# Kernel tuning notes

Hardware: AMD Instinct MI355X
Metric: run time of the kernel (lower is better)

Reference implementation:

```python
import math
import jax, jax.numpy as jnp
import numpy as np


def _bilinear_maps_sample(kv_feats, shapes_wh, start_ids, locs, map_ids):
    """Bilinear sampling from concatenated multi-level 2D maps.

    kv_feats: [BH, S, C] flattened (row-major, per level) feature maps
    shapes_wh: [L, 2] int (W, H) per level
    start_ids: [L] int start offset of each level in S
    locs: [BH, M, 2] normalized (x, y) in [0, 1]
    map_ids: [BH, M] int level index per sample
    returns [BH, M, C]
    """
    wh = shapes_wh[map_ids]                      # [BH, M, 2]
    W = wh[..., 0]
    H = wh[..., 1]
    start = start_ids[map_ids]                   # [BH, M]
    Wf = W.astype(locs.dtype)
    Hf = H.astype(locs.dtype)
    x = locs[..., 0] * Wf - 0.5                  # align_corners=False convention
    y = locs[..., 1] * Hf - 0.5
    x0 = jnp.floor(x)
    y0 = jnp.floor(y)
    out = jnp.zeros(locs.shape[:-1] + (kv_feats.shape[-1],), kv_feats.dtype)
    for dx in (0, 1):
        for dy in (0, 1):
            xi = x0 + dx
            yi = y0 + dy
            w = (1.0 - jnp.abs(x - xi)) * (1.0 - jnp.abs(y - yi))
            valid = (xi >= 0) & (xi < Wf) & (yi >= 0) & (yi < Hf)
            xi_c = jnp.clip(xi, 0, Wf - 1).astype(jnp.int32)
            yi_c = jnp.clip(yi, 0, Hf - 1).astype(jnp.int32)
            idx = start + yi_c * W + xi_c        # [BH, M]
            f = jnp.take_along_axis(kv_feats, idx[..., None], axis=1)
            out = out + jnp.where(valid, w, 0.0)[..., None] * f
    return out


def setup_inputs() -> dict:
    key = jax.random.key(0)
    ks = jax.random.split(key, 10)
    B, N, L, Hh, P = 2, 2048, 5, 8, 4
    in_size, sample_size = 256, 256
    qk_size, value_size = 256, 256
    kv_size = qk_size + value_size

    shapes = np.array([[128, 128], [64, 64], [32, 32], [16, 16], [8, 8]], np.int32)  # (H, W)
    flat = (shapes[:, 0] * shapes[:, 1]).astype(np.int64)
    start = np.concatenate([[0], np.cumsum(flat)[:-1]]).astype(np.int32)
    S = int(flat.sum())  # 21824

    # sampling_offsets bias: canonical Deformable-DETR grid init
    thetas = np.arange(Hh, dtype=np.float32) * (2.0 * math.pi / Hh)
    grid = np.stack([np.cos(thetas), np.sin(thetas)], axis=1)
    grid = grid / np.abs(grid).max(axis=1, keepdims=True)
    grid = np.tile(grid.reshape(Hh, 1, 1, 2), (1, L, 1, 1))
    sizes = np.arange(1, P + 1, dtype=np.float32).reshape(1, 1, P, 1)
    b_off = (sizes * grid).reshape(-1)           # [H*L*P*2]

    def lin(k, out_d, in_d):
        return jax.random.normal(k, (out_d, in_d), jnp.float32) * (1.0 / math.sqrt(in_d))

    return {
        "in_feats": jax.random.normal(ks[0], (B, N, in_size), jnp.float32),
        "sample_priors": jax.random.uniform(ks[1], (B, N, L, 2), jnp.float32),
        "sample_feats": jax.random.normal(ks[2], (B, S, sample_size), jnp.float32),
        "sample_map_shapes": jnp.asarray(shapes),
        "sample_map_start_ids": jnp.asarray(start),
        "W_off": jax.random.normal(ks[3], (Hh * L * P * 2, in_size), jnp.float32) * 0.02,
        "b_off": jnp.asarray(b_off),
        "W_q": lin(ks[4], qk_size, in_size),
        "b_q": jnp.zeros((qk_size,), jnp.float32),
        "W_kv": lin(ks[5], kv_size, sample_size),
        "b_kv": jnp.zeros((kv_size,), jnp.float32),
        "point_encs": jax.random.normal(ks[6], (Hh, L * P, qk_size // Hh), jnp.float32) * 0.02,
        "W_out": lin(ks[7], in_size, value_size),
        "b_out": jnp.zeros((in_size,), jnp.float32),
    }


def reference(in_feats, sample_priors, sample_feats, sample_map_shapes,
              sample_map_start_ids, W_off, b_off, W_q, b_q, W_kv, b_kv,
              point_encs, W_out, b_out):
    B, N = in_feats.shape[:2]
    Hh, LP, dqk = point_encs.shape
    L = sample_map_shapes.shape[0]
    P = LP // L

    # sampling offsets + locations (priors last dim == 2 path)
    off = (in_feats @ W_off.T + b_off).reshape(B, N, Hh, L, P, 2)
    shapes_wh = sample_map_shapes[:, ::-1]                      # fliplr -> (W, H)
    norm = shapes_wh.astype(in_feats.dtype)[None, None, None, :, None, :]
    locs = sample_priors[:, :, None, :, None, :] + off / norm    # [B,N,H,L,P,2]

    q = (in_feats @ W_q.T + b_q).reshape(B, N, Hh, dqk)
    kv = sample_feats @ W_kv.T + b_kv                            # [B,S,kv_size]
    ck = kv.shape[-1] // Hh
    kv = kv.reshape(B, -1, Hh, ck).transpose(0, 2, 1, 3).reshape(B * Hh, -1, ck)

    locs = locs.transpose(0, 2, 1, 3, 4, 5).reshape(B * Hh, N * L * P, 2)
    map_ids = jnp.broadcast_to(jnp.arange(L, dtype=jnp.int32)[None, None, :, None],
                               (B * Hh, N, L, P)).reshape(B * Hh, -1)

    sampled = _bilinear_maps_sample(kv, shapes_wh, sample_map_start_ids, locs, map_ids)
    sampled = sampled.reshape(B, Hh, N, LP, ck).transpose(0, 2, 1, 3, 4)  # [B,N,H,LP,ck]

    keys = sampled[..., :dqk] + point_encs                       # [B,N,H,LP,dqk]
    vals = sampled[..., dqk:]                                    # [B,N,H,LP,cv]
    attn = jax.nn.softmax(
        jnp.einsum('bnhd,bnhpd->bnhp', q / math.sqrt(dqk), keys), axis=-1)
    weighted = jnp.einsum('bnhp,bnhpd->bnhd', attn, vals).reshape(B, N, -1)
    return weighted @ W_out.T + b_out
```

## Files before the change

kernel.cpp:

```cpp
#include <hip/hip_runtime.h>
#include <cstddef>

#define B_  2
#define N_  2048
#define L_  5
#define HH  8
#define P_  4
#define S_  21824
#define DQK 32

using bf16x8 = __attribute__((ext_vector_type(8))) short;
using f32x4  = __attribute__((ext_vector_type(4))) float;
using us8    = __attribute__((ext_vector_type(8))) unsigned short;
using h2     = __attribute__((ext_vector_type(2))) _Float16;

__device__ __forceinline__ unsigned short f2b(float f) {
  unsigned u = __builtin_bit_cast(unsigned, f);
  u += 0x7FFFu + ((u >> 16) & 1u);
  return (unsigned short)(u >> 16);
}
__device__ __forceinline__ float b2f(unsigned short h) {
  return __builtin_bit_cast(float, ((unsigned)h) << 16);
}
__device__ __forceinline__ unsigned cvtpk(float lo, float hi) {
  unsigned r;
  asm("v_cvt_pk_bf16_f32 %0, %1, %2" : "=v"(r) : "v"(lo), "v"(hi));
  return r;
}
__device__ __forceinline__ h2 pkrtz(float a, float b) {
  return __builtin_bit_cast(h2, __builtin_amdgcn_cvt_pkrtz(a, b));
}
__device__ __forceinline__ unsigned pkrtz_u(float a, float b) {
  return __builtin_bit_cast(unsigned, __builtin_amdgcn_cvt_pkrtz(a, b));
}
__device__ __forceinline__ h2 u2h(unsigned u) { return __builtin_bit_cast(h2, u); }

__device__ __forceinline__ void gld_lds16(const void* g, void* l) {
  __builtin_amdgcn_global_load_lds(
      (const __attribute__((address_space(1))) unsigned int*)g,
      (__attribute__((address_space(3))) unsigned int*)l, 16, 0, 0);
}

template <int CTRL>
__device__ __forceinline__ float dppadd(float v) {
  const int x = __builtin_bit_cast(int, v);
  return v + __builtin_bit_cast(float,
      __builtin_amdgcn_update_dpp(x, x, CTRL, 0xF, 0xF, false));
}

#define F0 131072
#define F1 147456
#define F2 155648
#define F3 163840
#define F4 176128
#define F5 188416

__device__ __forceinline__ void cvt8_plain(const float* s, unsigned short* d, int u) {
  const float4 a = ((const float4*)s)[2 * u];
  const float4 b = ((const float4*)s)[2 * u + 1];
  us8 o;
  o[0] = f2b(a.x); o[1] = f2b(a.y); o[2] = f2b(a.z); o[3] = f2b(a.w);
  o[4] = f2b(b.x); o[5] = f2b(b.y); o[6] = f2b(b.z); o[7] = f2b(b.w);
  ((us8*)d)[u] = o;
}
__device__ __forceinline__ unsigned short f2b_lo(float x) {
  return f2b(x - b2f(f2b(x)));
}
__device__ __forceinline__ void cvt8_lo(const float* s, unsigned short* d, int u) {
  const float4 a = ((const float4*)s)[2 * u];
  const float4 b = ((const float4*)s)[2 * u + 1];
  us8 o;
  o[0] = f2b_lo(a.x); o[1] = f2b_lo(a.y); o[2] = f2b_lo(a.z); o[3] = f2b_lo(a.w);
  o[4] = f2b_lo(b.x); o[5] = f2b_lo(b.y); o[6] = f2b_lo(b.z); o[7] = f2b_lo(b.w);
  ((us8*)d)[u] = o;
}
__device__ __forceinline__ void cvt8_both(const float* s, unsigned short* dh,
                                          unsigned short* dl, int u) {
  const float4 a = ((const float4*)s)[2 * u];
  const float4 b = ((const float4*)s)[2 * u + 1];
  us8 oh, ol;
  const float v[8] = {a.x, a.y, a.z, a.w, b.x, b.y, b.z, b.w};
#pragma unroll
  for (int k = 0; k < 8; ++k) {
    const unsigned short hh = f2b(v[k]);
    oh[k] = hh;
    ol[k] = f2b(v[k] - b2f(hh));
  }
  ((us8*)dh)[u] = oh;
  ((us8*)dl)[u] = ol;
}

__global__ __launch_bounds__(256) void cvt_all(
    const float* __restrict__ in_feats, const float* __restrict__ W_kv,
    const float* __restrict__ W_q, const float* __restrict__ W_out,
    const float* __restrict__ W_off,
    unsigned short* __restrict__ if_hi, unsigned short* __restrict__ if_lo,
    unsigned short* __restrict__ wkv_bf, unsigned short* __restrict__ wq_bf,
    unsigned short* __restrict__ wout_bf, unsigned short* __restrict__ woff_hi,
    unsigned short* __restrict__ woff_lo) {
  const int i = blockIdx.x * 256 + threadIdx.x;
  if      (i < F0) cvt8_both(in_feats, if_hi, if_lo, i);
  else if (i < F1) cvt8_plain(W_kv, wkv_bf, i - F0);
  else if (i < F2) cvt8_plain(W_q, wq_bf, i - F1);
  else if (i < F3) cvt8_plain(W_out, wout_bf, i - F2);
  else if (i < F4) {
    const int u = i - F3;
    if ((u >> 5) < 320) cvt8_plain(W_off, woff_hi, u);
    else ((us8*)woff_hi)[u] = (us8)0;
  } else {
    const int u = i - F4;
    if ((u >> 5) < 320) cvt8_lo(W_off, woff_lo, u);
    else ((us8*)woff_lo)[u] = (us8)0;
  }
}

__device__ __forceinline__ void mfma_compute(
    const unsigned short* As, const unsigned short* Bs,
    int wr, int wc, int fr, int fq, f32x4 (&acc)[4][4]) {
#pragma unroll
  for (int kk = 0; kk < 2; ++kk) {
    bf16x8 af[4], bfv[4];
#pragma unroll
    for (int i = 0; i < 4; ++i) {
      const int ar = wr * 64 + i * 16 + fr;
      const int cha = (kk * 4 + fq) ^ (ar & 7);
      af[i] = *(const bf16x8*)(As + ar * 64 + cha * 8);
      const int br = wc * 64 + i * 16 + fr;
      const int chb = (kk * 4 + fq) ^ (br & 7);
      bfv[i] = *(const bf16x8*)(Bs + br * 64 + chb * 8);
    }
#pragma unroll
    for (int i = 0; i < 4; ++i)
#pragma unroll
      for (int j = 0; j < 4; ++j)
        acc[i][j] = __builtin_amdgcn_mfma_f32_16x16x32_bf16(
            af[i], bfv[j], acc[i][j], 0, 0, 0);
  }
}

__device__ __forceinline__ void mfma_tile_bf16(
    const unsigned short* __restrict__ Ap, const unsigned short* __restrict__ Wp,
    unsigned short* As, unsigned short* Bs,
    int row0, int col0, int wv, int wr, int wc, int fr, int fq,
    int srow, int sch, f32x4 (&acc)[4][4]) {
  for (int k0 = 0; k0 < 256; k0 += 64) {
#pragma unroll
    for (int i = 0; i < 4; ++i) {
      const int r = i * 32 + srow;
      const int ca = sch ^ (r & 7);
      gld_lds16(Ap + (size_t)(row0 + r) * 256 + k0 + ca * 8,
                As + (size_t)(i * 32 + wv * 8) * 64);
      gld_lds16(Wp + (size_t)(col0 + r) * 256 + k0 + ca * 8,
                Bs + (size_t)(i * 32 + wv * 8) * 64);
    }
    __syncthreads();
    mfma_compute(As, Bs, wr, wc, fr, fq, acc);
    __syncthreads();
  }
}

__global__ __launch_bounds__(256) void ubergemm(
    const float* __restrict__ sfeats,
    const unsigned short* __restrict__ wkv_bf,
    const unsigned short* __restrict__ if_hi,
    const unsigned short* __restrict__ if_lo,
    const unsigned short* __restrict__ woff_hi,
    const unsigned short* __restrict__ woff_lo,
    const unsigned short* __restrict__ wq_bf,
    const float* __restrict__ b_kv, const float* __restrict__ b_off,
    const float* __restrict__ b_q,
    unsigned short* __restrict__ kvt, float* __restrict__ offb,
    float* __restrict__ qb) {
  __shared__ __align__(16) unsigned char ldsraw[49152];

  const int tid = threadIdx.x;
  const int lane = tid & 63;
  const int wv = tid >> 6;
  const int wr = wv >> 1, wc = wv & 1;
  const int fr = lane & 15, fq = lane >> 4;
  const int bx = blockIdx.x;

  f32x4 acc[4][4] = {};

  if (bx >= 160) {
    const int t = bx - 160;
    const int x = t & 7;
    const int idx = t >> 3;
    const int c = idx & 3;
    const int g = (idx >> 2) * 8 + x;
    if (g >= 341) return;
    const int row0 = g * 128;
    const int col0 = c * 128;

    float* Afb[2] = {(float*)ldsraw, (float*)(ldsraw + 16384)};
    unsigned short* Bb[2] = {(unsigned short*)(ldsraw + 32768),
                             (unsigned short*)(ldsraw + 40960)};

#define KV_STAGE(KK, BUF)                                                     \
    {                                                                         \
      _Pragma("unroll")                                                       \
      for (int ld = 0; ld < 4; ++ld) {             \
        const int ci = ld * 256 + tid;                                        \
        const int rw = ci >> 3, cc = ci & 7;                                  \
        const int ca = cc ^ (rw & 7);                                         \
        gld_lds16(sfeats + (size_t)(row0 + rw) * 256 + (KK) * 32 + ca * 4,    \
                  (char*)Afb[BUF] + (ld * 4096 + wv * 1024));                 \
      }                                                                       \
      _Pragma("unroll")                                                       \
      for (int ld = 0; ld < 2; ++ld) {              \
        const int ci = ld * 256 + tid;                                        \
        const int rw = ci >> 2, cc = ci & 3;                                  \
        const int ca = cc ^ ((rw >> 1) & 3);        \
        gld_lds16(wkv_bf + (size_t)(col0 + rw) * 256 + (KK) * 32 + ca * 8,    \
                  (char*)Bb[BUF] + (ld * 4096 + wv * 1024));                  \
      }                                                                       \
    }

    KV_STAGE(0, 0);
#pragma unroll
    for (int k = 0; k < 8; ++k) {
      if (k < 7) {
        KV_STAGE(k + 1, (k + 1) & 1);
        asm volatile("s_waitcnt vmcnt(6)" ::: "memory");
      } else {
        asm volatile("s_waitcnt vmcnt(0)" ::: "memory");
      }
      __builtin_amdgcn_s_barrier();
      __builtin_amdgcn_sched_barrier(0);
      const float* Ac = Afb[k & 1];
      const unsigned short* Bc = Bb[k & 1];
      bf16x8 af[4], bfv[4];
#pragma unroll
      for (int i = 0; i < 4; ++i) {
        const int ar = wr * 64 + i * 16 + fr;
        const int swz = ar & 7;
        const float4 a0 = *(const float4*)(Ac + ar * 32 + (((fq * 2) ^ swz) * 4));
        const float4 a1 = *(const float4*)(Ac + ar * 32 + (((fq * 2 + 1) ^ swz) * 4));
        uint4 u;
        u.x = cvtpk(a0.x, a0.y);
        u.y = cvtpk(a0.z, a0.w);
        u.z = cvtpk(a1.x, a1.y);
        u.w = cvtpk(a1.z, a1.w);
        af[i] = __builtin_bit_cast(bf16x8, u);
      }
#pragma unroll
      for (int j = 0; j < 4; ++j) {
        const int nr = wc * 64 + j * 16 + fr;
        bfv[j] = *(const bf16x8*)(Bc + (nr * 4 + (fq ^ ((nr >> 1) & 3))) * 8);
      }
      __builtin_amdgcn_s_setprio(1);
#pragma unroll
      for (int j = 0; j < 4; ++j)
#pragma unroll
        for (int i = 0; i < 4; ++i)
          acc[j][i] = __builtin_amdgcn_mfma_f32_16x16x32_bf16(
              bfv[j], af[i], acc[j][i], 0, 0, 0);
      __builtin_amdgcn_s_setprio(0);
      __builtin_amdgcn_s_barrier();
    }
#undef KV_STAGE

#pragma unroll
    for (int j = 0; j < 4; ++j) {
      const int c0 = col0 + wc * 64 + j * 16 + fq * 4;
      const float4 bb = *(const float4*)(b_kv + c0);
      const int h = c0 >> 6;
      const int cc = c0 & 63;
#pragma unroll
      for (int i = 0; i < 4; ++i) {
        const int sl = row0 + wr * 64 + i * 16 + fr;
        const int b = (sl >= S_) ? 1 : 0;
        const int s = sl - b * S_;
        unsigned* dst = (unsigned*)(kvt + ((size_t)(b * HH + h) * S_ + s) * 64 + cc);
        dst[0] = pkrtz_u(acc[j][i][0] + bb.x, acc[j][i][1] + bb.y);
        dst[1] = pkrtz_u(acc[j][i][2] + bb.z, acc[j][i][3] + bb.w);
      }
    }
    return;
  }

  unsigned short* As = (unsigned short*)ldsraw;
  unsigned short* Bs = (unsigned short*)(ldsraw + 16384);
  const int srow = tid >> 3;
  const int sch = tid & 7;
  int row0, col0, ldc, nbias;
  const float* bias;
  float* Cf;
  if (bx < 96) {
    col0 = (bx % 3) * 128; row0 = (bx / 3) * 128;
    bias = b_off; Cf = offb; ldc = 384; nbias = 320;
    mfma_tile_bf16(if_hi, woff_hi, As, Bs, row0, col0, wv, wr, wc, fr, fq, srow, sch, acc);
    mfma_tile_bf16(if_hi, woff_lo, As, Bs, row0, col0, wv, wr, wc, fr, fq, srow, sch, acc);
    mfma_tile_bf16(if_lo, woff_hi, As, Bs, row0, col0, wv, wr, wc, fr, fq, srow, sch, acc);
  } else {
    const int t = bx - 96;
    col0 = (t & 1) * 128; row0 = (t >> 1) * 128;
    bias = b_q; Cf = qb; ldc = 256; nbias = 256;
    mfma_tile_bf16(if_hi, wq_bf, As, Bs, row0, col0, wv, wr, wc, fr, fq, srow, sch, acc);
  }

#pragma unroll
  for (int j = 0; j < 4; ++j) {
    const int n = col0 + wc * 64 + j * 16 + fr;
    const float bv = (n < nbias) ? bias[n] : 0.f;
#pragma unroll
    for (int i = 0; i < 4; ++i) {
      const int mbase = row0 + wr * 64 + i * 16 + fq * 4;
#pragma unroll
      for (int r = 0; r < 4; ++r)
        Cf[(size_t)(mbase + r) * ldc + n] = acc[i][j][r] + bv;
    }
  }
}

__global__ __launch_bounds__(256) void gemm_out(
    const unsigned short* __restrict__ A, const unsigned short* __restrict__ Wt,
    const float* __restrict__ bias, float* __restrict__ C) {
  __shared__ __align__(16) unsigned short As[128 * 64];
  __shared__ __align__(16) unsigned short Bs[128 * 64];
  const int tid = threadIdx.x;
  const int lane = tid & 63;
  const int wv = tid >> 6;
  const int wr = wv >> 1, wc = wv & 1;
  const int fr = lane & 15, fq = lane >> 4;
  const int row0 = blockIdx.y * 128, col0 = blockIdx.x * 128;
  const int srow = tid >> 3, sch = tid & 7;
  f32x4 acc[4][4] = {};
  mfma_tile_bf16(A, Wt, As, Bs, row0, col0, wv, wr, wc, fr, fq, srow, sch, acc);
#pragma unroll
  for (int j = 0; j < 4; ++j) {
    const int n = col0 + wc * 64 + j * 16 + fr;
    const float bv = bias[n];
#pragma unroll
    for (int i = 0; i < 4; ++i) {
      const int mbase = row0 + wr * 64 + i * 16 + fq * 4;
#pragma unroll
      for (int r = 0; r < 4; ++r)
        C[(size_t)(mbase + r) * 256 + n] = acc[i][j][r] + bv;
    }
  }
}

__global__ __launch_bounds__(256) void sample_attn6(
    const unsigned short* __restrict__ kvt,
    const float* __restrict__ offb,
    const float* __restrict__ qb,
    const float* __restrict__ priors,
    const int* __restrict__ shapes,
    const int* __restrict__ starts,
    const float* __restrict__ pencs,
    unsigned short* __restrict__ wtd) {
  __shared__ __align__(16) int pbuf[4][20][8];
  const int wv = threadIdx.x >> 6;
  const int lane = threadIdx.x & 63;
  const int beta = blockIdx.x;
  const int sig = (beta & 7) * 2 + (beta >> 12);
  const int chunk = (beta >> 3) & 511;
  const int h = sig & 7;
  const int b = sig >> 3;
  const int bn = b * N_ + chunk * 4 + wv;
  const int j = lane & 31;
  const int half = lane >> 5;

  if (lane < 20) {
    const int pp = lane;
    const int l = pp >> 2;
    const float2 oxy = *(const float2*)(offb + (size_t)bn * 384 + h * 40 + pp * 2);
    const float2 pxy = *(const float2*)(priors + ((size_t)bn * 5 + l) * 2);
    const int Wd = shapes[l * 2 + 1];
    const int Hd = shapes[l * 2 + 0];
    const int st = starts[l];
    const float Wf = (float)Wd, Hf = (float)Hd;
    const float x = (pxy.x + oxy.x / Wf) * Wf - 0.5f;
    const float y = (pxy.y + oxy.y / Hf) * Hf - 0.5f;
    const float x0f = floorf(x), y0f = floorf(y);
    const float fx = x - x0f, fy = y - y0f;
    const int xi = (int)x0f, yi = (int)y0f;
    int a[4]; unsigned wpk[4];
#pragma unroll
    for (int dy = 0; dy < 2; ++dy)
#pragma unroll
      for (int dx = 0; dx < 2; ++dx) {
        const int xc = xi + dx, yc = yi + dy;
        const bool valid = (xc >= 0) & (xc < Wd) & (yc >= 0) & (yc < Hd);
        const float wt = (dx ? fx : 1.f - fx) * (dy ? fy : 1.f - fy);
        const float wm = valid ? wt : 0.f;
        const int xcc = min(max(xc, 0), Wd - 1);
        const int ycc = min(max(yc, 0), Hd - 1);
        a[dy * 2 + dx] = (st + ycc * Wd + xcc) * 32;
        wpk[dy * 2 + dx] = pkrtz_u(wm, wm);
      }
    *(int4*)&pbuf[wv][pp][0] = make_int4(a[0], a[1], a[2], a[3]);
    *(int4*)&pbuf[wv][pp][4] =
        make_int4((int)wpk[0], (int)wpk[1], (int)wpk[2], (int)wpk[3]);
  }

  const int jc = j & 15;
  float2 q2 = *(const float2*)(qb + (size_t)bn * 256 + h * DQK + 2 * jc);
  q2.x *= 0.17677669529663687f;
  q2.y *= 0.17677669529663687f;
  const h2 qpk = pkrtz(q2.x, q2.y);
  float qpe[10];
#pragma unroll
  for (int i = 0; i < 10; ++i) {
    const float2 pe = *(const float2*)(
        pencs + ((size_t)h * 20 + 2 * i + half) * DQK + 2 * jc);
    qpe[i] = q2.x * pe.x + q2.y * pe.y;
  }

  const unsigned* kvd = (const unsigned*)(kvt + (size_t)(b * HH + h) * (S_ * 64));

  uint4 wwp[5];
  unsigned g[5][4];
#pragma unroll
  for (int i = 0; i < 5; ++i) {
    const int4 aa = *(const int4*)&pbuf[wv][2 * i + half][0];
    wwp[i] = *(const uint4*)&pbuf[wv][2 * i + half][4];
    g[i][0] = kvd[(unsigned)aa.x + j];
    g[i][1] = kvd[(unsigned)aa.y + j];
    g[i][2] = kvd[(unsigned)aa.z + j];
    g[i][3] = kvd[(unsigned)aa.w + j];
  }

  h2 sam[10];
  float lg[10];
#pragma unroll
  for (int i = 0; i < 10; ++i) {
    const int s = i % 5;
    const uint4 wt = wwp[s];
    const unsigned g0 = g[s][0], g1 = g[s][1], g2 = g[s][2], g3 = g[s][3];
    if (i < 5) {
      const int4 aa = *(const int4*)&pbuf[wv][2 * (i + 5) + half][0];
      wwp[s] = *(const uint4*)&pbuf[wv][2 * (i + 5) + half][4];
      g[s][0] = kvd[(unsigned)aa.x + j];
      g[s][1] = kvd[(unsigned)aa.y + j];
      g[s][2] = kvd[(unsigned)aa.z + j];
      g[s][3] = kvd[(unsigned)aa.w + j];
    }
    h2 v = u2h(wt.x) * u2h(g0);
    v = u2h(wt.y) * u2h(g1) + v;
    v = u2h(wt.z) * u2h(g2) + v;
    v = u2h(wt.w) * u2h(g3) + v;
    sam[i] = v;
    float part = (j < 16) ? __builtin_amdgcn_fdot2(qpk, v, qpe[i], false) : 0.f;
    part = dppadd<0xB1>(part);
    part = dppadd<0x4E>(part);
    part = dppadd<0x124>(part);
    part = dppadd<0x128>(part);
    lg[i] = part + __shfl_xor(part, 16, 64);
  }

  float mx = lg[0];
#pragma unroll
  for (int i = 1; i < 10; ++i) mx = fmaxf(mx, lg[i]);
  mx = fmaxf(mx, __shfl_xor(mx, 32, 64));
  float se = 0.f;
#pragma unroll
  for (int i = 0; i < 10; ++i) {
    lg[i] = __expf(lg[i] - mx);
    se += lg[i];
  }
  se += __shfl_xor(se, 32, 64);
  const float inv = 1.f / se;

  float ax = 0.f, ay = 0.f;
#pragma unroll
  for (int i = 0; i < 10; ++i) {
    ax = fmaf(lg[i], (float)sam[i][0], ax);
    ay = fmaf(lg[i], (float)sam[i][1], ay);
  }
  ax += __shfl_xor(ax, 32, 64);
  ay += __shfl_xor(ay, 32, 64);

  if (half == 0 && j >= 16) {
    const unsigned u = (unsigned)f2b(ax * inv) | ((unsigned)f2b(ay * inv) << 16);
    ((unsigned*)wtd)[(size_t)bn * 128 + h * 16 + (j - 16)] = u;
  }
}

extern "C" void kernel_launch(void* const* d_in, const int* in_sizes, int n_in,
                              void* d_out, int out_size, void* d_ws, size_t ws_size,
                              hipStream_t stream) {
  const float* in_feats = (const float*)d_in[0];
  const float* priors   = (const float*)d_in[1];
  const float* sfeats   = (const float*)d_in[2];
  const int*   shapes   = (const int*)d_in[3];
  const int*   starts   = (const int*)d_in[4];
  const float* W_off    = (const float*)d_in[5];
  const float* b_off    = (const float*)d_in[6];
  const float* W_q      = (const float*)d_in[7];
  const float* b_q      = (const float*)d_in[8];
  const float* W_kv     = (const float*)d_in[9];
  const float* b_kv     = (const float*)d_in[10];
  const float* pencs    = (const float*)d_in[11];
  const float* W_out    = (const float*)d_in[12];
  const float* b_out    = (const float*)d_in[13];
  float* out = (float*)d_out;

  char* w = (char*)d_ws;
  unsigned short* kvt = (unsigned short*)w;
  w += (size_t)B_ * HH * S_ * 64 * 2;
  unsigned short* if_hi = (unsigned short*)w; w += (size_t)4096 * 256 * 2;
  unsigned short* if_lo = (unsigned short*)w; w += (size_t)4096 * 256 * 2;
  unsigned short* wkv_bf = (unsigned short*)w;  w += (size_t)512 * 256 * 2;
  unsigned short* wq_bf  = (unsigned short*)w;  w += (size_t)256 * 256 * 2;
  unsigned short* wout_bf = (unsigned short*)w; w += (size_t)256 * 256 * 2;
  unsigned short* woff_hi = (unsigned short*)w; w += (size_t)384 * 256 * 2;
  unsigned short* woff_lo = (unsigned short*)w; w += (size_t)384 * 256 * 2;
  float* offb = (float*)w;  w += (size_t)4096 * 384 * 4;
  float* qb   = (float*)w;  w += (size_t)4096 * 256 * 4;
  unsigned short* wtd_bf = (unsigned short*)w; w += (size_t)4096 * 256 * 2;

  cvt_all<<<F5 / 256, 256, 0, stream>>>(
      in_feats, W_kv, W_q, W_out, W_off,
      if_hi, if_lo, wkv_bf, wq_bf, wout_bf, woff_hi, woff_lo);

  ubergemm<<<1536, 256, 0, stream>>>(
      sfeats, wkv_bf, if_hi, if_lo, woff_hi, woff_lo, wq_bf,
      b_kv, b_off, b_q, kvt, offb, qb);

  sample_attn6<<<(B_ * N_ * HH) / 4, 256, 0, stream>>>(
      kvt, offb, qb, priors, shapes, starts, pencs, wtd_bf);

  gemm_out<<<dim3(2, 32), 256, 0, stream>>>(wtd_bf, wout_bf, b_out, out);
}
```

Measured before the change: 82.00 us.

## Stage KV GEMM A operand through registers as bf16 in LDS

The fp32 source features for the KV projection are now loaded into registers, converted to bf16 once per element, and written swizzled into LDS, instead of being copied to LDS as fp32 and converted by every wave that reads them. This halves the A-tile LDS footprint, shrinking total shared memory from 48KB to 32KB, and an occupancy hint of 4 blocks per CU is added. In exchange the A loads lose async direct-to-LDS overlap, and a full vmcnt/lgkmcnt wait before each barrier may expose global load latency.

```diff
diff --git a/kernel.cpp b/kernel.cpp
--- a/kernel.cpp
+++ b/kernel.cpp
@@ -159,7 +159,7 @@
   }
 }
 
-__global__ __launch_bounds__(256) void ubergemm(
+__global__ __launch_bounds__(256, 4) void ubergemm(
     const float* __restrict__ sfeats,
     const unsigned short* __restrict__ wkv_bf,
     const unsigned short* __restrict__ if_hi,
@@ -171,7 +171,7 @@
     const float* __restrict__ b_q,
     unsigned short* __restrict__ kvt, float* __restrict__ offb,
     float* __restrict__ qb) {
-  __shared__ __align__(16) unsigned char ldsraw[49152];
+  __shared__ __align__(16) unsigned char ldsraw[32768];
 
   const int tid = threadIdx.x;
   const int lane = tid & 63;
@@ -192,56 +192,65 @@
     const int row0 = g * 128;
     const int col0 = c * 128;
 
-    float* Afb[2] = {(float*)ldsraw, (float*)(ldsraw + 16384)};
-    unsigned short* Bb[2] = {(unsigned short*)(ldsraw + 32768),
-                             (unsigned short*)(ldsraw + 40960)};
-
-#define KV_STAGE(KK, BUF)                                                     \
+    unsigned short* Ab[2] = {(unsigned short*)ldsraw,
+                             (unsigned short*)(ldsraw + 8192)};
+    unsigned short* Bb[2] = {(unsigned short*)(ldsraw + 16384),
+                             (unsigned short*)(ldsraw + 24576)};
+
+    const int ci0 = tid, ci1 = 256 + tid;
+    const int rw0 = ci0 >> 2, cc0 = ci0 & 3;
+    const int rw1 = ci1 >> 2, cc1 = ci1 & 3;
+    const float* a0p = sfeats + (size_t)(row0 + rw0) * 256 + cc0 * 8;
+    const float* a1p = sfeats + (size_t)(row0 + rw1) * 256 + cc1 * 8;
+    unsigned short* aw0 = nullptr; unsigned short* aw1 = nullptr;
+
+#define KV_STAGE_B(KK, BUF)                                                   \
     {                                                                         \
       _Pragma("unroll")                                                       \
-      for (int ld = 0; ld < 4; ++ld) {             \
-        const int ci = ld * 256 + tid;                                        \
-        const int rw = ci >> 3, cc = ci & 7;                                  \
-        const int ca = cc ^ (rw & 7);                                         \
-        gld_lds16(sfeats + (size_t)(row0 + rw) * 256 + (KK) * 32 + ca * 4,    \
-                  (char*)Afb[BUF] + (ld * 4096 + wv * 1024));                 \
-      }                                                                       \
-      _Pragma("unroll")                                                       \
-      for (int ld = 0; ld < 2; ++ld) {              \
+      for (int ld = 0; ld < 2; ++ld) {                                        \
         const int ci = ld * 256 + tid;                                        \
         const int rw = ci >> 2, cc = ci & 3;                                  \
-        const int ca = cc ^ ((rw >> 1) & 3);        \
+        const int ca = cc ^ ((rw >> 1) & 3);                                  \
         gld_lds16(wkv_bf + (size_t)(col0 + rw) * 256 + (KK) * 32 + ca * 8,    \
                   (char*)Bb[BUF] + (ld * 4096 + wv * 1024));                  \
       }                                                                       \
     }
 
-    KV_STAGE(0, 0);
+    float4 ar0a, ar0b, ar1a, ar1b;
+    ar0a = *(const float4*)(a0p + 0 * 32);
+    ar0b = *(const float4*)(a0p + 0 * 32 + 4);
+    ar1a = *(const float4*)(a1p + 0 * 32);
+    ar1b = *(const float4*)(a1p + 0 * 32 + 4);
+    KV_STAGE_B(0, 0);
+    {
+      uint4 u0, u1;
+      u0.x = cvtpk(ar0a.x, ar0a.y); u0.y = cvtpk(ar0a.z, ar0a.w);
+      u0.z = cvtpk(ar0b.x, ar0b.y); u0.w = cvtpk(ar0b.z, ar0b.w);
+      u1.x = cvtpk(ar1a.x, ar1a.y); u1.y = cvtpk(ar1a.z, ar1a.w);
+      u1.z = cvtpk(ar1b.x, ar1b.y); u1.w = cvtpk(ar1b.z, ar1b.w);
+      *(uint4*)(Ab[0] + (rw0 * 4 + (cc0 ^ ((rw0 >> 1) & 3))) * 8) = u0;
+      *(uint4*)(Ab[0] + (rw1 * 4 + (cc1 ^ ((rw1 >> 1) & 3))) * 8) = u1;
+    }
+    __syncthreads();
+
 #pragma unroll
     for (int k = 0; k < 8; ++k) {
       if (k < 7) {
-        KV_STAGE(k + 1, (k + 1) & 1);
-        asm volatile("s_waitcnt vmcnt(6)" ::: "memory");
-      } else {
-        asm volatile("s_waitcnt vmcnt(0)" ::: "memory");
+        ar0a = *(const float4*)(a0p + (k + 1) * 32);
+        ar0b = *(const float4*)(a0p + (k + 1) * 32 + 4);
+        ar1a = *(const float4*)(a1p + (k + 1) * 32);
+        ar1b = *(const float4*)(a1p + (k + 1) * 32 + 4);
+        KV_STAGE_B(k + 1, (k + 1) & 1);
+        aw0 = Ab[(k + 1) & 1] + (rw0 * 4 + (cc0 ^ ((rw0 >> 1) & 3))) * 8;
+        aw1 = Ab[(k + 1) & 1] + (rw1 * 4 + (cc1 ^ ((rw1 >> 1) & 3))) * 8;
       }
-      __builtin_amdgcn_s_barrier();
-      __builtin_amdgcn_sched_barrier(0);
-      const float* Ac = Afb[k & 1];
+      const unsigned short* Ac = Ab[k & 1];
       const unsigned short* Bc = Bb[k & 1];
       bf16x8 af[4], bfv[4];
 #pragma unroll
       for (int i = 0; i < 4; ++i) {
         const int ar = wr * 64 + i * 16 + fr;
-        const int swz = ar & 7;
-        const float4 a0 = *(const float4*)(Ac + ar * 32 + (((fq * 2) ^ swz) * 4));
-        const float4 a1 = *(const float4*)(Ac + ar * 32 + (((fq * 2 + 1) ^ swz) * 4));
-        uint4 u;
-        u.x = cvtpk(a0.x, a0.y);
-        u.y = cvtpk(a0.z, a0.w);
-        u.z = cvtpk(a1.x, a1.y);
-        u.w = cvtpk(a1.z, a1.w);
-        af[i] = __builtin_bit_cast(bf16x8, u);
+        af[i] = *(const bf16x8*)(Ac + (ar * 4 + (fq ^ ((ar >> 1) & 3))) * 8);
       }
 #pragma unroll
       for (int j = 0; j < 4; ++j) {
@@ -256,9 +265,19 @@
           acc[j][i] = __builtin_amdgcn_mfma_f32_16x16x32_bf16(
               bfv[j], af[i], acc[j][i], 0, 0, 0);
       __builtin_amdgcn_s_setprio(0);
+      if (k < 7) {
+        uint4 u0, u1;
+        u0.x = cvtpk(ar0a.x, ar0a.y); u0.y = cvtpk(ar0a.z, ar0a.w);
+        u0.z = cvtpk(ar0b.x, ar0b.y); u0.w = cvtpk(ar0b.z, ar0b.w);
+        u1.x = cvtpk(ar1a.x, ar1a.y); u1.y = cvtpk(ar1a.z, ar1a.w);
+        u1.z = cvtpk(ar1b.x, ar1b.y); u1.w = cvtpk(ar1b.z, ar1b.w);
+        *(uint4*)aw0 = u0;
+        *(uint4*)aw1 = u1;
+        asm volatile("s_waitcnt vmcnt(0) lgkmcnt(0)" ::: "memory");
+      }
       __builtin_amdgcn_s_barrier();
     }
-#undef KV_STAGE
+#undef KV_STAGE_B
 
 #pragma unroll
     for (int j = 0; j < 4; ++j) {
```

Result: slower. 86.01 us (+4.9%).
